# Optimization experiments

Measured on AMD Instinct MI355X. Metric: run time of the kernel, lower is better.

## Reference

```python
import jax, jax.numpy as jnp
import numpy as np

N = 20000       # nodes
E = 320000      # edges
IN_C = 256      # in_channels
HID = 256       # hidden_channels
H = 8           # heads
D = HID // H    # head dim = 32
SCALE = 1.0 / np.sqrt(D)
DIN = IN_C + HID


def _lin_params(key, din, dout):
    k1, k2 = jax.random.split(key)
    W = jax.random.normal(k1, (din, dout), jnp.float32) * (1.0 / np.sqrt(din))
    b = jax.random.normal(k2, (dout,), jnp.float32) * 0.01
    return W, b


def setup_inputs() -> dict:
    key = jax.random.key(0)
    ks = jax.random.split(key, 16)
    inp = {
        "x": jax.random.normal(ks[0], (N, IN_C), jnp.float32),
        "h": jax.random.normal(ks[1], (N, HID), jnp.float32) * 0.1,
        "edge_index": jax.random.randint(ks[2], (2, E), 0, N, dtype=jnp.int32),
    }
    i = 3
    for name in ["z", "r", "c"]:
        for p in ["Wq", "Wk", "Wv", "Ws"]:
            W, b = _lin_params(ks[i], DIN, HID)
            i += 1
            inp[f"{name}_{p}"] = W
            inp[f"{name}_b{p[1].lower()}"] = b
    return inp


def _tconv(x, src, dst, Wq, bq, Wk, bk, Wv, bv, Ws, bs):
    """PyG TransformerConv (eval mode, concat=True, root_weight=True, beta=False)."""
    # dense per-node projections, then edge-indexed gathers
    q = (x @ Wq + bq)[dst].reshape(-1, H, D)   # [E, H, D] query at target
    k = (x @ Wk + bk)[src].reshape(-1, H, D)   # [E, H, D] key at source
    v = (x @ Wv + bv)[src].reshape(-1, H, D)   # [E, H, D] value at source
    logits = jnp.sum(q * k, axis=-1) * SCALE   # [E, H]
    # segment softmax over each destination's neighborhood
    m = jax.ops.segment_max(logits, dst, num_segments=N)
    e = jnp.exp(logits - m[dst])
    s = jax.ops.segment_sum(e, dst, num_segments=N)
    alpha = e / (s[dst] + 1e-16)               # [E, H]
    agg = jax.ops.segment_sum(alpha[:, :, None] * v, dst, num_segments=N)
    return agg.reshape(N, HID) + x @ Ws + bs   # attention out + root skip


def reference(x, h, edge_index,
              z_Wq, z_bq, z_Wk, z_bk, z_Wv, z_bv, z_Ws, z_bs,
              r_Wq, r_bq, r_Wk, r_bk, r_Wv, r_bv, r_Ws, r_bs,
              c_Wq, c_bq, c_Wk, c_bk, c_Wv, c_bv, c_Ws, c_bs):
    src, dst = edge_index[0], edge_index[1]
    h_in = jnp.concatenate([x, h], axis=-1)                      # [N, DIN]
    z = jax.nn.sigmoid(_tconv(h_in, src, dst, z_Wq, z_bq, z_Wk, z_bk, z_Wv, z_bv, z_Ws, z_bs))
    r = jax.nn.sigmoid(_tconv(h_in, src, dst, r_Wq, r_bq, r_Wk, r_bk, r_Wv, r_bv, r_Ws, r_bs))
    h_cand = jnp.concatenate([x, r * h], axis=-1)                # [N, DIN]
    h_tilde = jnp.tanh(_tconv(h_cand, src, dst, c_Wq, c_bq, c_Wk, c_bk, c_Wv, c_bv, c_Ws, c_bs))
    return z * h + (1.0 - z) * h_tilde
```

## Files before the change

### kernel.cpp

```cpp
#include <hip/hip_runtime.h>
#include <hip/hip_bf16.h>
#include <math.h>

#define NNODES 20000
#define MPAD 20096
#define NEDGES 320000
#define HIDC 256
#define DINC 512
#define NHEAD 8
#define HDIM 32
#define SCALE 0.17677669529663687f
#define ZRCHUNK 16
#define CCHUNK 32

typedef __attribute__((ext_vector_type(8))) short short8;
typedef __attribute__((ext_vector_type(4))) float f32x4;

__device__ __forceinline__ void gload_lds16(const void* g, void* l) {
    __builtin_amdgcn_global_load_lds(
        (const __attribute__((address_space(1))) unsigned int*)g,
        (__attribute__((address_space(3))) unsigned int*)l, 16, 0, 0);
}

__device__ __forceinline__ float bfbits(unsigned short u) {
    return __uint_as_float(((unsigned)u) << 16);
}

__global__ __launch_bounds__(256) void concat_xh(const float* __restrict__ x,
                                                 const float* __restrict__ h,
                                                 __hip_bfloat16* __restrict__ out) {
    int i = blockIdx.x * 256 + threadIdx.x;
    int total = MPAD * DINC;
    if (i >= total) return;
    int row = i >> 9;
    int col = i & 511;
    float v = 0.f;
    if (row < NNODES)
        v = (col < HIDC) ? x[row * HIDC + col] : h[row * HIDC + (col - HIDC)];
    out[i] = __float2bfloat16(v);
}

struct WPtrs { const float* p[12]; };

__global__ __launch_bounds__(256) void transpose_w(WPtrs wp, __hip_bfloat16* __restrict__ out) {
    __shared__ float t[64][65];
    int mat = blockIdx.z;
    int kt = blockIdx.x * 64;
    int nt = blockIdx.y * 64;
    const float* W = wp.p[mat];
    int c = threadIdx.x & 63, r4 = threadIdx.x >> 6;
#pragma unroll
    for (int rr = 0; rr < 16; ++rr) {
        int k_l = r4 + rr * 4;
        t[k_l][c] = W[(kt + k_l) * HIDC + nt + c];
    }
    __syncthreads();
#pragma unroll
    for (int rr = 0; rr < 16; ++rr) {
        int n_l = r4 + rr * 4;
        out[mat * (HIDC * DINC) + (nt + n_l) * DINC + kt + c] =
            __float2bfloat16(t[c][n_l]);
    }
}

__global__ __launch_bounds__(256) void count_deg(const int* __restrict__ dst,
                                                 int* __restrict__ deg) {
    int e = blockIdx.x * 256 + threadIdx.x;
    if (e >= NEDGES) return;
    atomicAdd(&deg[dst[e]], 1);
}

__global__ __launch_bounds__(1024) void exscan(const int* __restrict__ deg,
                                               int* __restrict__ rowptr,
                                               int* __restrict__ pos) {
    __shared__ int sdata[1024];
    __shared__ int s_carry;
    const int tid = threadIdx.x;
    if (tid == 0) { s_carry = 0; rowptr[0] = 0; }
    __syncthreads();
    for (int base = 0; base < NNODES; base += 1024) {
        int i = base + tid;
        int v = (i < NNODES) ? deg[i] : 0;
        sdata[tid] = v;
        __syncthreads();
        for (int off = 1; off < 1024; off <<= 1) {
            int t = (tid >= off) ? sdata[tid - off] : 0;
            __syncthreads();
            sdata[tid] += t;
            __syncthreads();
        }
        int incl = sdata[tid];
        int carry = s_carry;
        if (i < NNODES) {
            int ex = carry + incl - v;
            rowptr[i] = ex;
            pos[i] = ex;
            if (i == NNODES - 1) rowptr[NNODES] = carry + incl;
        }
        __syncthreads();
        if (tid == 1023) s_carry = carry + incl;
        __syncthreads();
    }
}

__global__ __launch_bounds__(256) void scatter_src(const int* __restrict__ src,
                                                   const int* __restrict__ dst,
                                                   int* __restrict__ pos,
                                                   int* __restrict__ csrc) {
    int e = blockIdx.x * 256 + threadIdx.x;
    if (e >= NEDGES) return;
    int idx = atomicAdd(&pos[dst[e]], 1);
    csrc[idx] = src[e];
}

struct GemmArgs { const float* bias[8]; void* C[8]; unsigned bf16mask; };

template <int NZ>
__global__ __launch_bounds__(256) void gemm_mfma(
    const __hip_bfloat16* __restrict__ A,
    const __hip_bfloat16* __restrict__ WtBase,
    GemmArgs ga) {
    __shared__ __align__(16) char smem[2][32768];

    int nwg = gridDim.x;
    int per = nwg >> 3;
    int lin = (blockIdx.x & 7) * per + (blockIdx.x >> 3);
    int bmIdx = lin / NZ;
    int nz = lin % NZ;
    int bm = bmIdx * 128;
    int bn = (nz & 1) * 128;
    int z = nz >> 1;

    const __hip_bfloat16* Bt = WtBase + (size_t)z * (HIDC * DINC);
    const float* bias = ga.bias[z];
    void* Cv = ga.C[z];
    bool isb = (ga.bf16mask >> z) & 1;

    int tid = threadIdx.x;
    int wave = tid >> 6, lane = tid & 63;
    int lrow = lane >> 3;
    int lcol = (lane & 7) ^ lrow;

    int wr = wave >> 1, wc = wave & 1;
    int m_base = wr * 64, n_base = wc * 64;
    int l16 = lane & 15, lk = lane >> 4;

    f32x4 acc[4][4] = {};

    auto stage = [&](int buf, int kt) {
        char* As = smem[buf];
        char* Bs = smem[buf] + 16384;
#pragma unroll
        for (int c4 = 0; c4 < 4; ++c4) {
            int c = wave * 4 + c4;
            gload_lds16(&A[(size_t)(bm + c * 8 + lrow) * DINC + kt + lcol * 8],
                        As + c * 1024);
        }
#pragma unroll
        for (int c4 = 0; c4 < 4; ++c4) {
            int c = wave * 4 + c4;
            gload_lds16(&Bt[(size_t)(bn + c * 8 + lrow) * DINC + kt + lcol * 8],
                        Bs + c * 1024);
        }
    };

    auto compute = [&](int buf) {
        char* As = smem[buf];
        char* Bs = smem[buf] + 16384;
#pragma unroll
        for (int kk = 0; kk < 2; ++kk) {
            short8 af[4], bf[4];
#pragma unroll
            for (int f = 0; f < 4; ++f) {
                int row = m_base + f * 16 + l16;
                int lin2 = row * 128 + (kk * 32 + lk * 8) * 2;
                af[f] = *(const short8*)(As + (lin2 ^ ((row & 7) << 4)));
                int rowb = n_base + f * 16 + l16;
                int linb = rowb * 128 + (kk * 32 + lk * 8) * 2;
                bf[f] = *(const short8*)(Bs + (linb ^ ((rowb & 7) << 4)));
            }
#pragma unroll
            for (int i = 0; i < 4; ++i)
#pragma unroll
                for (int j = 0; j < 4; ++j)
                    acc[i][j] = __builtin_amdgcn_mfma_f32_16x16x32_bf16(
                        af[i], bf[j], acc[i][j], 0, 0, 0);
        }
    };

    stage(0, 0);
#pragma unroll
    for (int t = 0; t < 8; ++t) {
        int cur = t & 1;
        if (t < 7) {
            stage(cur ^ 1, (t + 1) * 64);
            asm volatile("s_waitcnt vmcnt(8)" ::: "memory");
        } else {
            asm volatile("s_waitcnt vmcnt(0)" ::: "memory");
        }
        __builtin_amdgcn_s_barrier();
        __builtin_amdgcn_sched_barrier(0);
        compute(cur);
        __builtin_amdgcn_sched_barrier(0);
        __builtin_amdgcn_s_barrier();
    }

#pragma unroll
    for (int i = 0; i < 4; ++i) {
#pragma unroll
        for (int j = 0; j < 4; ++j) {
            int n = bn + n_base + j * 16 + l16;
            float bia = bias[n];
#pragma unroll
            for (int r = 0; r < 4; ++r) {
                int m = bm + m_base + i * 16 + lk * 4 + r;
                if (m < NNODES) {
                    float val = acc[i][j][r] + bia;
                    if (isb)
                        ((__hip_bfloat16*)Cv)[(size_t)m * HIDC + n] = __float2bfloat16(val);
                    else
                        ((float*)Cv)[(size_t)m * HIDC + n] = val;
                }
            }
        }
    }
}

__global__ __launch_bounds__(256) void attn_zr(
    const __hip_bfloat16* __restrict__ Qz, const __hip_bfloat16* __restrict__ Kz,
    const __hip_bfloat16* __restrict__ Vz, const float* __restrict__ Sz,
    const __hip_bfloat16* __restrict__ Qr, const __hip_bfloat16* __restrict__ Kr,
    const __hip_bfloat16* __restrict__ Vr, const float* __restrict__ Sr,
    const int* __restrict__ rowptr, const int* __restrict__ csrc,
    const float* __restrict__ h,
    float* __restrict__ Zout, __hip_bfloat16* __restrict__ abuf) {
    int node = blockIdx.x;
    int t = threadIdx.x;
    int eL = t >> 4;
    int gA = (t >> 3) & 1;
    int hL = t & 7;
    int gC = t >> 7;
    int u = t & 127;
    int hC = u >> 4;

    __shared__ int sn_lds[ZRCHUNK];
    __shared__ float w_lds[2][ZRCHUNK][8];

    const __hip_bfloat16* Qa = gA ? Qr : Qz;
    const __hip_bfloat16* Ka = gA ? Kr : Kz;
    const __hip_bfloat16* Vc = gC ? Vr : Vz;

    float qreg[32];
    {
        const short8* Qrow = (const short8*)&Qa[(size_t)node * HIDC + hL * 32];
#pragma unroll
        for (int i = 0; i < 4; ++i) {
            short8 v = Qrow[i];
#pragma unroll
            for (int j = 0; j < 8; ++j)
                qreg[i * 8 + j] = bfbits((unsigned short)v[j]);
        }
    }

    int beg = rowptr[node], end = rowptr[node + 1];
    float acc0 = 0.f, acc1 = 0.f, s_priv = 0.f;

    for (int base = beg; base < end; base += ZRCHUNK) {
        int cnt = min(ZRCHUNK, end - base);
        __syncthreads();
        if (t < cnt) sn_lds[t] = csrc[base + t];
        __syncthreads();
        if (eL < cnt) {
            int sn = sn_lds[eL];
            const short8* Krow = (const short8*)&Ka[(size_t)sn * HIDC + hL * 32];
            float dot = 0.f;
#pragma unroll
            for (int i = 0; i < 4; ++i) {
                short8 kv = Krow[i];
#pragma unroll
                for (int j = 0; j < 8; ++j)
                    dot += qreg[i * 8 + j] * bfbits((unsigned short)kv[j]);
            }
            w_lds[gA][eL][hL] = __expf(dot * SCALE);
        }
        __syncthreads();
#pragma unroll 4
        for (int e = 0; e < cnt; ++e) {
            int sn = sn_lds[e];
            float w = w_lds[gC][e][hC];
            unsigned pv = *(const unsigned*)&Vc[(size_t)sn * HIDC + 2 * u];
            acc0 += w * __uint_as_float((pv & 0xffffu) << 16);
            acc1 += w * __uint_as_float(pv & 0xffff0000u);
            s_priv += w;
        }
    }

    float inv = 1.f / (s_priv + 1e-16f);
    int c0 = 2 * u;
    const float* Sx = gC ? Sr : Sz;
    float p0 = acc0 * inv + Sx[(size_t)node * HIDC + c0];
    float p1 = acc1 * inv + Sx[(size_t)node * HIDC + c0 + 1];
    float g0 = 1.f / (1.f + __expf(-p0));
    float g1 = 1.f / (1.f + __expf(-p1));
    if (gC == 0) {
        Zout[(size_t)node * HIDC + c0] = g0;
        Zout[(size_t)node * HIDC + c0 + 1] = g1;
    } else {
        float h0 = h[(size_t)node * HIDC + c0];
        float h1 = h[(size_t)node * HIDC + c0 + 1];
        abuf[(size_t)node * DINC + HIDC + c0] = __float2bfloat16(g0 * h0);
        abuf[(size_t)node * DINC + HIDC + c0 + 1] = __float2bfloat16(g1 * h1);
    }
}

__global__ __launch_bounds__(256) void attn_c(
    const __hip_bfloat16* __restrict__ Q, const __hip_bfloat16* __restrict__ K,
    const __hip_bfloat16* __restrict__ V, const float* __restrict__ S,
    const int* __restrict__ rowptr, const int* __restrict__ csrc,
    const float* __restrict__ zbuf, const float* __restrict__ h,
    float* __restrict__ out) {
    int node = blockIdx.x;
    int t = threadIdx.x;
    int eL = t >> 3, hL = t & 7;
    int c = t, hC = t >> 5;

    __shared__ int sn_lds[CCHUNK];
    __shared__ float w_lds[CCHUNK][8];

    float qreg[32];
    {
        const short8* Qrow = (const short8*)&Q[(size_t)node * HIDC + hL * 32];
#pragma unroll
        for (int i = 0; i < 4; ++i) {
            short8 v = Qrow[i];
#pragma unroll
            for (int j = 0; j < 8; ++j)
                qreg[i * 8 + j] = bfbits((unsigned short)v[j]);
        }
    }

    int beg = rowptr[node], end = rowptr[node + 1];
    float acc = 0.f, s_priv = 0.f;

    for (int base = beg; base < end; base += CCHUNK) {
        int cnt = min(CCHUNK, end - base);
        __syncthreads();
        if (t < cnt) sn_lds[t] = csrc[base + t];
        __syncthreads();
        if (eL < cnt) {
            int sn = sn_lds[eL];
            const short8* Krow = (const short8*)&K[(size_t)sn * HIDC + hL * 32];
            float dot = 0.f;
#pragma unroll
            for (int i = 0; i < 4; ++i) {
                short8 kv = Krow[i];
#pragma unroll
                for (int j = 0; j < 8; ++j)
                    dot += qreg[i * 8 + j] * bfbits((unsigned short)kv[j]);
            }
            w_lds[eL][hL] = __expf(dot * SCALE);
        }
        __syncthreads();
#pragma unroll 4
        for (int e = 0; e < cnt; ++e) {
            int sn = sn_lds[e];
            float w = w_lds[e][hC];
            acc += w * __bfloat162float(V[(size_t)sn * HIDC + c]);
            s_priv += w;
        }
    }

    float agg = acc / (s_priv + 1e-16f);
    float pre = agg + S[(size_t)node * HIDC + c];
    float ht = tanhf(pre);
    float zz = zbuf[(size_t)node * HIDC + c];
    float hh = h[(size_t)node * HIDC + c];
    out[(size_t)node * HIDC + c] = zz * hh + (1.f - zz) * ht;
}

extern "C" void kernel_launch(void* const* d_in, const int* in_sizes, int n_in,
                              void* d_out, int out_size, void* d_ws, size_t ws_size,
                              hipStream_t stream) {
    const float* x = (const float*)d_in[0];
    const float* h = (const float*)d_in[1];
    const int* ei = (const int*)d_in[2];
    const float* Wf[3][4];
    const float* B[3][4];
    for (int g = 0; g < 3; ++g)
        for (int p = 0; p < 4; ++p) {
            Wf[g][p] = (const float*)d_in[3 + g * 8 + p * 2];
            B[g][p] = (const float*)d_in[3 + g * 8 + p * 2 + 1];
        }

    char* ws = (char*)d_ws;
    size_t off = 0;
    auto alloc = [&](size_t bytes) {
        void* p = ws + off;
        off = (off + bytes + 255) & ~(size_t)255;
        return p;
    };
    __hip_bfloat16* Abuf = (__hip_bfloat16*)alloc((size_t)MPAD * DINC * 2);
    __hip_bfloat16* Wt = (__hip_bfloat16*)alloc((size_t)12 * HIDC * DINC * 2);
    __hip_bfloat16* Qz = (__hip_bfloat16*)alloc((size_t)NNODES * HIDC * 2);
    __hip_bfloat16* Kz = (__hip_bfloat16*)alloc((size_t)NNODES * HIDC * 2);
    __hip_bfloat16* Vz = (__hip_bfloat16*)alloc((size_t)NNODES * HIDC * 2);
    float* Sz = (float*)alloc((size_t)NNODES * HIDC * 4);
    __hip_bfloat16* Qr = (__hip_bfloat16*)alloc((size_t)NNODES * HIDC * 2);
    __hip_bfloat16* Kr = (__hip_bfloat16*)alloc((size_t)NNODES * HIDC * 2);
    __hip_bfloat16* Vr = (__hip_bfloat16*)alloc((size_t)NNODES * HIDC * 2);
    float* Sr = (float*)alloc((size_t)NNODES * HIDC * 4);
    float* Zb = (float*)alloc((size_t)NNODES * HIDC * 4);
    int* deg = (int*)alloc((size_t)NNODES * 4);
    int* rowptr = (int*)alloc((size_t)(NNODES + 1) * 4);
    int* pos = (int*)alloc((size_t)NNODES * 4);
    int* csrc = (int*)alloc((size_t)NEDGES * 4);

    const int* srcArr = ei;
    const int* dstArr = ei + NEDGES;

    WPtrs wp;
    for (int g = 0; g < 3; ++g)
        for (int p = 0; p < 4; ++p) wp.p[g * 4 + p] = Wf[g][p];

    hipMemsetAsync(deg, 0, NNODES * sizeof(int), stream);
    concat_xh<<<(MPAD * DINC + 255) / 256, 256, 0, stream>>>(x, h, Abuf);
    transpose_w<<<dim3(8, 4, 12), 256, 0, stream>>>(wp, Wt);
    count_deg<<<(NEDGES + 255) / 256, 256, 0, stream>>>(dstArr, deg);
    exscan<<<1, 1024, 0, stream>>>(deg, rowptr, pos);
    scatter_src<<<(NEDGES + 255) / 256, 256, 0, stream>>>(srcArr, dstArr, pos, csrc);

    {
        GemmArgs ga;
        for (int p = 0; p < 4; ++p) { ga.bias[p] = B[0][p]; ga.bias[4 + p] = B[1][p]; }
        ga.C[0] = Qz; ga.C[1] = Kz; ga.C[2] = Vz; ga.C[3] = Sz;
        ga.C[4] = Qr; ga.C[5] = Kr; ga.C[6] = Vr; ga.C[7] = Sr;
        ga.bf16mask = 0x77;
        gemm_mfma<16><<<(MPAD / 128) * 16, 256, 0, stream>>>(Abuf, Wt, ga);
    }
    attn_zr<<<NNODES, 256, 0, stream>>>(Qz, Kz, Vz, Sz, Qr, Kr, Vr, Sr,
                                        rowptr, csrc, h, Zb, Abuf);
    {
        GemmArgs ga;
        for (int p = 0; p < 8; ++p) { ga.bias[p] = B[2][p & 3]; ga.C[p] = nullptr; }
        for (int p = 0; p < 4; ++p) ga.bias[p] = B[2][p];
        ga.C[0] = Qz; ga.C[1] = Kz; ga.C[2] = Vz; ga.C[3] = Sz;
        ga.bf16mask = 0x7;
        gemm_mfma<8><<<(MPAD / 128) * 8, 256, 0, stream>>>(
            Abuf, Wt + (size_t)8 * HIDC * DINC, ga);
    }
    attn_c<<<NNODES, 256, 0, stream>>>(Qz, Kz, Vz, Sz, rowptr, csrc,
                                       Zb, h, (float*)d_out);
}
```

Before: 418.2 us.

## Map one wavefront per node in attention kernels using shuffles instead of LDS

Both attention kernels now assign a single 64-lane wavefront to each destination node, packing four nodes per block, instead of a whole 256-thread block per node. Neighbor indices and softmax weights are exchanged with wave shuffles, so the LDS staging and block-wide barriers are gone. Each lane now accumulates 8 (z/r) or 4 (c) channels with wider vector loads of V. The aim is to cut synchronization overhead and idle threads on low-degree nodes, at the cost of smaller per-iteration edge chunks and more serial work per lane.

```diff
diff --git a/kernel.cpp b/kernel.cpp
--- a/kernel.cpp
+++ b/kernel.cpp
@@ -10,10 +10,9 @@
 #define NHEAD 8
 #define HDIM 32
 #define SCALE 0.17677669529663687f
-#define ZRCHUNK 16
-#define CCHUNK 32
 
 typedef __attribute__((ext_vector_type(8))) short short8;
+typedef __attribute__((ext_vector_type(4))) short svec4;
 typedef __attribute__((ext_vector_type(4))) float f32x4;
 
 __device__ __forceinline__ void gload_lds16(const void* g, void* l) {
@@ -234,17 +233,17 @@
     const int* __restrict__ rowptr, const int* __restrict__ csrc,
     const float* __restrict__ h,
     float* __restrict__ Zout, __hip_bfloat16* __restrict__ abuf) {
-    int node = blockIdx.x;
-    int t = threadIdx.x;
-    int eL = t >> 4;
-    int gA = (t >> 3) & 1;
-    int hL = t & 7;
-    int gC = t >> 7;
-    int u = t & 127;
-    int hC = u >> 4;
-
-    __shared__ int sn_lds[ZRCHUNK];
-    __shared__ float w_lds[2][ZRCHUNK][8];
+    int lane = threadIdx.x & 63;
+    int node = blockIdx.x * 4 + (threadIdx.x >> 6);
+
+    int eA = lane >> 4;
+    int gA = (lane >> 3) & 1;
+    int hA = lane & 7;
+    int gC = lane >> 5;
+    int cL = lane & 31;
+    int cBase = cL * 8;
+    int hC = cL >> 2;
+    int wsrc = gC * 8 + hC;
 
     const __hip_bfloat16* Qa = gA ? Qr : Qz;
     const __hip_bfloat16* Ka = gA ? Kr : Kz;
@@ -252,7 +251,7 @@
 
     float qreg[32];
     {
-        const short8* Qrow = (const short8*)&Qa[(size_t)node * HIDC + hL * 32];
+        const short8* Qrow = (const short8*)&Qa[(size_t)node * HIDC + hA * 32];
 #pragma unroll
         for (int i = 0; i < 4; ++i) {
             short8 v = Qrow[i];
@@ -263,16 +262,17 @@
     }
 
     int beg = rowptr[node], end = rowptr[node + 1];
-    float acc0 = 0.f, acc1 = 0.f, s_priv = 0.f;
-
-    for (int base = beg; base < end; base += ZRCHUNK) {
-        int cnt = min(ZRCHUNK, end - base);
-        __syncthreads();
-        if (t < cnt) sn_lds[t] = csrc[base + t];
-        __syncthreads();
-        if (eL < cnt) {
-            int sn = sn_lds[eL];
-            const short8* Krow = (const short8*)&Ka[(size_t)sn * HIDC + hL * 32];
+    float acc[8] = {};
+    float s_priv = 0.f;
+
+    for (int base = beg; base < end; base += 4) {
+        int cnt = min(4, end - base);
+        int sn = 0;
+        if (lane < cnt) sn = csrc[base + lane];
+        int mySn = __shfl(sn, eA);
+        float w = 0.f;
+        if (eA < cnt) {
+            const short8* Krow = (const short8*)&Ka[(size_t)mySn * HIDC + hA * 32];
             float dot = 0.f;
 #pragma unroll
             for (int i = 0; i < 4; ++i) {
@@ -281,35 +281,36 @@
                 for (int j = 0; j < 8; ++j)
                     dot += qreg[i * 8 + j] * bfbits((unsigned short)kv[j]);
             }
-            w_lds[gA][eL][hL] = __expf(dot * SCALE);
-        }
-        __syncthreads();
+            w = __expf(dot * SCALE);
+        }
 #pragma unroll 4
         for (int e = 0; e < cnt; ++e) {
-            int sn = sn_lds[e];
-            float w = w_lds[gC][e][hC];
-            unsigned pv = *(const unsigned*)&Vc[(size_t)sn * HIDC + 2 * u];
-            acc0 += w * __uint_as_float((pv & 0xffffu) << 16);
-            acc1 += w * __uint_as_float(pv & 0xffff0000u);
-            s_priv += w;
+            int sne = __shfl(sn, e);
+            float we = __shfl(w, e * 16 + wsrc);
+            short8 v = *(const short8*)&Vc[(size_t)sne * HIDC + cBase];
+#pragma unroll
+            for (int j = 0; j < 8; ++j) acc[j] += we * bfbits((unsigned short)v[j]);
+            s_priv += we;
         }
     }
 
     float inv = 1.f / (s_priv + 1e-16f);
-    int c0 = 2 * u;
     const float* Sx = gC ? Sr : Sz;
-    float p0 = acc0 * inv + Sx[(size_t)node * HIDC + c0];
-    float p1 = acc1 * inv + Sx[(size_t)node * HIDC + c0 + 1];
-    float g0 = 1.f / (1.f + __expf(-p0));
-    float g1 = 1.f / (1.f + __expf(-p1));
+    float g[8];
+#pragma unroll
+    for (int j = 0; j < 8; ++j) {
+        float p = acc[j] * inv + Sx[(size_t)node * HIDC + cBase + j];
+        g[j] = 1.f / (1.f + __expf(-p));
+    }
     if (gC == 0) {
-        Zout[(size_t)node * HIDC + c0] = g0;
-        Zout[(size_t)node * HIDC + c0 + 1] = g1;
+        float* Zp = &Zout[(size_t)node * HIDC + cBase];
+#pragma unroll
+        for (int j = 0; j < 8; ++j) Zp[j] = g[j];
     } else {
-        float h0 = h[(size_t)node * HIDC + c0];
-        float h1 = h[(size_t)node * HIDC + c0 + 1];
-        abuf[(size_t)node * DINC + HIDC + c0] = __float2bfloat16(g0 * h0);
-        abuf[(size_t)node * DINC + HIDC + c0 + 1] = __float2bfloat16(g1 * h1);
+        const float* hp = &h[(size_t)node * HIDC + cBase];
+        __hip_bfloat16* ap = &abuf[(size_t)node * DINC + HIDC + cBase];
+#pragma unroll
+        for (int j = 0; j < 8; ++j) ap[j] = __float2bfloat16(g[j] * hp[j]);
     }
 }
 
@@ -319,17 +320,17 @@
     const int* __restrict__ rowptr, const int* __restrict__ csrc,
     const float* __restrict__ zbuf, const float* __restrict__ h,
     float* __restrict__ out) {
-    int node = blockIdx.x;
-    int t = threadIdx.x;
-    int eL = t >> 3, hL = t & 7;
-    int c = t, hC = t >> 5;
-
-    __shared__ int sn_lds[CCHUNK];
-    __shared__ float w_lds[CCHUNK][8];
+    int lane = threadIdx.x & 63;
+    int node = blockIdx.x * 4 + (threadIdx.x >> 6);
+
+    int eA = lane >> 3;
+    int hA = lane & 7;
+    int cBase = lane * 4;
+    int hC = lane >> 3;
 
     float qreg[32];
     {
-        const short8* Qrow = (const short8*)&Q[(size_t)node * HIDC + hL * 32];
+        const short8* Qrow = (const short8*)&Q[(size_t)node * HIDC + hA * 32];
 #pragma unroll
         for (int i = 0; i < 4; ++i) {
             short8 v = Qrow[i];
@@ -340,16 +341,17 @@
     }
 
     int beg = rowptr[node], end = rowptr[node + 1];
-    float acc = 0.f, s_priv = 0.f;
-
-    for (int base = beg; base < end; base += CCHUNK) {
-        int cnt = min(CCHUNK, end - base);
-        __syncthreads();
-        if (t < cnt) sn_lds[t] = csrc[base + t];
-        __syncthreads();
-        if (eL < cnt) {
-            int sn = sn_lds[eL];
-            const short8* Krow = (const short8*)&K[(size_t)sn * HIDC + hL * 32];
+    float acc[4] = {};
+    float s_priv = 0.f;
+
+    for (int base = beg; base < end; base += 8) {
+        int cnt = min(8, end - base);
+        int sn = 0;
+        if (lane < cnt) sn = csrc[base + lane];
+        int mySn = __shfl(sn, eA);
+        float w = 0.f;
+        if (eA < cnt) {
+            const short8* Krow = (const short8*)&K[(size_t)mySn * HIDC + hA * 32];
             float dot = 0.f;
 #pragma unroll
             for (int i = 0; i < 4; ++i) {
@@ -358,24 +360,30 @@
                 for (int j = 0; j < 8; ++j)
                     dot += qreg[i * 8 + j] * bfbits((unsigned short)kv[j]);
             }
-            w_lds[eL][hL] = __expf(dot * SCALE);
-        }
-        __syncthreads();
+            w = __expf(dot * SCALE);
+        }
 #pragma unroll 4
         for (int e = 0; e < cnt; ++e) {
-            int sn = sn_lds[e];
-            float w = w_lds[e][hC];
-            acc += w * __bfloat162float(V[(size_t)sn * HIDC + c]);
-            s_priv += w;
-        }
-    }
-
-    float agg = acc / (s_priv + 1e-16f);
-    float pre = agg + S[(size_t)node * HIDC + c];
-    float ht = tanhf(pre);
-    float zz = zbuf[(size_t)node * HIDC + c];
-    float hh = h[(size_t)node * HIDC + c];
-    out[(size_t)node * HIDC + c] = zz * hh + (1.f - zz) * ht;
+            int sne = __shfl(sn, e);
+            float we = __shfl(w, e * 8 + hC);
+            svec4 v = *(const svec4*)&V[(size_t)sne * HIDC + cBase];
+#pragma unroll
+            for (int j = 0; j < 4; ++j) acc[j] += we * bfbits((unsigned short)v[j]);
+            s_priv += we;
+        }
+    }
+
+    float inv = 1.f / (s_priv + 1e-16f);
+    f32x4 o;
+#pragma unroll
+    for (int j = 0; j < 4; ++j) {
+        float pre = acc[j] * inv + S[(size_t)node * HIDC + cBase + j];
+        float ht = tanhf(pre);
+        float zz = zbuf[(size_t)node * HIDC + cBase + j];
+        float hh = h[(size_t)node * HIDC + cBase + j];
+        o[j] = zz * hh + (1.f - zz) * ht;
+    }
+    *(f32x4*)&out[(size_t)node * HIDC + cBase] = o;
 }
 
 extern "C" void kernel_launch(void* const* d_in, const int* in_sizes, int n_in,
@@ -422,7 +430,7 @@
     for (int g = 0; g < 3; ++g)
         for (int p = 0; p < 4; ++p) wp.p[g * 4 + p] = Wf[g][p];
 
-    hipMemsetAsync(deg, 0, NNODES * sizeof(int), stream);
+    (void)hipMemsetAsync(deg, 0, NNODES * sizeof(int), stream);
     concat_xh<<<(MPAD * DINC + 255) / 256, 256, 0, stream>>>(x, h, Abuf);
     transpose_w<<<dim3(8, 4, 12), 256, 0, stream>>>(wp, Wt);
     count_deg<<<(NEDGES + 255) / 256, 256, 0, stream>>>(dstArr, deg);
@@ -437,17 +445,16 @@
         ga.bf16mask = 0x77;
         gemm_mfma<16><<<(MPAD / 128) * 16, 256, 0, stream>>>(Abuf, Wt, ga);
     }
-    attn_zr<<<NNODES, 256, 0, stream>>>(Qz, Kz, Vz, Sz, Qr, Kr, Vr, Sr,
-                                        rowptr, csrc, h, Zb, Abuf);
+    attn_zr<<<NNODES / 4, 256, 0, stream>>>(Qz, Kz, Vz, Sz, Qr, Kr, Vr, Sr,
+                                            rowptr, csrc, h, Zb, Abuf);
     {
         GemmArgs ga;
         for (int p = 0; p < 8; ++p) { ga.bias[p] = B[2][p & 3]; ga.C[p] = nullptr; }
-        for (int p = 0; p < 4; ++p) ga.bias[p] = B[2][p];
         ga.C[0] = Qz; ga.C[1] = Kz; ga.C[2] = Vz; ga.C[3] = Sz;
         ga.bf16mask = 0x7;
         gemm_mfma<8><<<(MPAD / 128) * 8, 256, 0, stream>>>(
             Abuf, Wt + (size_t)8 * HIDC * DINC, ga);
     }
-    attn_c<<<NNODES, 256, 0, stream>>>(Qz, Kz, Vz, Sz, rowptr, csrc,
-                                       Zb, h, (float*)d_out);
-}
+    attn_c<<<NNODES / 4, 256, 0, stream>>>(Qz, Kz, Vz, Sz, rowptr, csrc,
+                                           Zb, h, (float*)d_out);
+}
```

New measurement: 418.0 us. Within noise of the previous version (-0.0%).
